# Kernel tuning notes

Measured on AMD Instinct MI355X. Metric: run time of the kernel, lower is better.

The kernel has to match this reference:

```python
import jax, jax.numpy as jnp
import numpy as np

D_MODEL = 1024
N_HEAD = 16
D_HEAD = D_MODEL // N_HEAD
BSZ, QLEN, MLEN = 2, 1024, 1024
KLEN = QLEN + MLEN


def setup_inputs() -> dict:
    key = jax.random.key(0)
    ks = jax.random.split(key, 10)
    s = 1.0 / np.sqrt(D_MODEL)
    inp = {
        "x": jax.random.normal(ks[0], (BSZ, QLEN, D_MODEL), jnp.float32),
        "mem": jax.random.normal(ks[1], (BSZ, MLEN, D_MODEL), jnp.float32),
        "pos_emb": jax.random.normal(ks[2], (KLEN, D_MODEL), jnp.float32),
        # causal mask with memory: query i may attend to key j iff j <= i + MLEN
        "attn_mask": (jnp.arange(KLEN)[None, :] > (jnp.arange(QLEN)[:, None] + MLEN))[None, None],
        "Wq": jax.random.normal(ks[3], (D_MODEL, D_MODEL), jnp.float32) * s,
        "Wk": jax.random.normal(ks[4], (D_MODEL, D_MODEL), jnp.float32) * s,
        "Wv": jax.random.normal(ks[5], (D_MODEL, D_MODEL), jnp.float32) * s,
        "Wr": jax.random.normal(ks[6], (D_MODEL, D_MODEL), jnp.float32) * s,
        "Wo": jax.random.normal(ks[7], (D_MODEL, D_MODEL), jnp.float32) * s,
        "r_w_bias": jax.random.normal(ks[8], (N_HEAD, D_HEAD), jnp.float32) * 0.02,
        "r_r_bias": jax.random.normal(ks[9], (N_HEAD, D_HEAD), jnp.float32) * 0.02,
    }
    return inp


def _rel_shift(x):
    # x: [b, n, q, k]
    b, n, q, k = x.shape
    x_padded = jnp.pad(x, ((0, 0), (0, 0), (0, 0), (1, 0)))  # zero column at front
    x_padded = x_padded.reshape(b, n, k + 1, q)
    return x_padded[:, :, 1:].reshape(b, n, q, k)


def reference(x, mem, pos_emb, attn_mask, Wq, Wk, Wv, Wr, Wo, r_w_bias, r_r_bias):
    bsz, qlen, _ = x.shape
    k_input = jnp.concatenate([mem, x], axis=1)
    klen = k_input.shape[1]
    scale = 1.0 / np.sqrt(D_HEAD)

    # projections -> [b, n, len, d]
    q = jnp.einsum('bqe,de->bqd', x, Wq).reshape(bsz, qlen, N_HEAD, D_HEAD).transpose(0, 2, 1, 3)
    k = jnp.einsum('bke,de->bkd', k_input, Wk).reshape(bsz, klen, N_HEAD, D_HEAD).transpose(0, 2, 1, 3)
    v = jnp.einsum('bke,de->bkd', k_input, Wv).reshape(bsz, klen, N_HEAD, D_HEAD).transpose(0, 2, 1, 3)
    r = jnp.einsum('ke,de->kd', pos_emb, Wr).reshape(klen, N_HEAD, D_HEAD).transpose(1, 0, 2)  # [n,k,d]

    AC = jnp.einsum('bnqd,bnkd->bnqk', q + r_w_bias[None, :, None, :], k)
    BD = jnp.einsum('bnqd,nkd->bnqk', q + r_r_bias[None, :, None, :], r)
    BD = _rel_shift(BD)

    attn_score = (AC + BD) * scale
    attn_score = jnp.where(attn_mask, -jnp.inf, attn_score)
    attn_prob = jax.nn.softmax(attn_score, axis=-1)

    attn_vec = jnp.einsum('bnqk,bnkd->bnqd', attn_prob, v)
    attn_vec = attn_vec.transpose(0, 2, 1, 3).reshape(bsz, qlen, N_HEAD * D_HEAD)
    return jnp.einsum('bqd,ed->bqe', attn_vec, Wo)
```

## Files before the change

kernel.cpp:

```cpp
#include <hip/hip_runtime.h>


#define B_SZ 2
#define QLEN 1024
#define MLEN 1024
#define KLEN 2048
#define DMODEL 1024
#define NH 16
#define DH 64

typedef _Float16 f16;
typedef __attribute__((ext_vector_type(8))) _Float16 f16x8;
typedef __attribute__((ext_vector_type(4))) _Float16 f16x4;
typedef __attribute__((ext_vector_type(4))) float f32x4;

__device__ __forceinline__ f16 f2h(float v) { return (f16)v; }
__device__ __forceinline__ float h2f(f16 v) { return (float)v; }

__device__ __forceinline__ f32x4 mfma16(f16x8 a, f16x8 b, f32x4 c) {
  return __builtin_amdgcn_mfma_f32_16x16x32_f16(a, b, c, 0, 0, 0);
}

__device__ __forceinline__ void gload_lds16(const f16* g, f16* l) {
  __builtin_amdgcn_global_load_lds(
      (const __attribute__((address_space(1))) void*)g,
      (__attribute__((address_space(3))) void*)l, 16, 0, 0);
}

__device__ __forceinline__ float bperm(int srclane, float v) {
  return __int_as_float(
      __builtin_amdgcn_ds_bpermute(srclane << 2, __float_as_int(v)));
}

__global__ __launch_bounds__(256) void convert_kernel(const float* __restrict__ src,
                                                      f16* __restrict__ dst, int n4) {
  const int i = blockIdx.x * 256 + threadIdx.x;
  if (i >= n4) return;
  const float4 v = reinterpret_cast<const float4*>(src)[i];
  f16x4 o = {(f16)v.x, (f16)v.y, (f16)v.z, (f16)v.w};
  reinterpret_cast<f16x4*>(dst)[i] = o;
}

__global__ __launch_bounds__(256) void pack_weights_kernel(
    const float* __restrict__ Wq, const float* __restrict__ Wk,
    const float* __restrict__ Wv, const float* __restrict__ Wr,
    const float* __restrict__ Wo, f16* __restrict__ Wqb, f16* __restrict__ Wkb,
    f16* __restrict__ Wvb, f16* __restrict__ Wrb, f16* __restrict__ Wob) {
  const float* src;
  f16* dst;
  switch (blockIdx.y) {
    case 0: src = Wq; dst = Wqb; break;
    case 1: src = Wk; dst = Wkb; break;
    case 2: src = Wv; dst = Wvb; break;
    case 3: src = Wr; dst = Wrb; break;
    default: src = Wo; dst = Wob; break;
  }
  const int i = blockIdx.x * 256 + threadIdx.x;
  const float4 v = reinterpret_cast<const float4*>(src)[i];
  f16x4 o = {(f16)v.x, (f16)v.y, (f16)v.z, (f16)v.w};
  reinterpret_cast<f16x4*>(dst)[i] = o;
}

__global__ __launch_bounds__(256) void build_kin_kernel(const float* __restrict__ x,
                                                        const float* __restrict__ mem,
                                                        f16* __restrict__ kin,
                                                        f16* __restrict__ xb) {
  const int i = blockIdx.x * 256 + threadIdx.x;
  const int per_b = KLEN * DMODEL / 4;
  const int b = i / per_b;
  const int rem = i - b * per_b;
  const int row = rem / (DMODEL / 4);
  const int cc = (rem - row * (DMODEL / 4)) * 4;
  const float* src = (row < MLEN)
      ? mem + ((size_t)b * MLEN + row) * DMODEL + cc
      : x + ((size_t)b * QLEN + (row - MLEN)) * DMODEL + cc;
  const float4 v = *reinterpret_cast<const float4*>(src);
  f16x4 o = {(f16)v.x, (f16)v.y, (f16)v.z, (f16)v.w};
  *reinterpret_cast<f16x4*>(kin + (size_t)i * 4) = o;
  if (row >= MLEN)
    *reinterpret_cast<f16x4*>(&xb[((size_t)b * QLEN + (row - MLEN)) * DMODEL + cc]) = o;
}

template <int DUAL, int OUT_F32>
__device__ __forceinline__ void gemm_core(const f16* __restrict__ A,
                                          const f16* __restrict__ Bm,
                                          void* __restrict__ C0v,
                                          void* __restrict__ C1v,
                                          const float* __restrict__ bias0,
                                          const float* __restrict__ bias1, int bm,
                                          int bn) {
  const int tid = threadIdx.x;
  const int wave = tid >> 6, lane = tid & 63;
  const int wr = wave >> 1, wc = wave & 1;
  const int lr = lane & 15, hi = lane >> 4;

  __shared__ f16 As[128 * 64];
  __shared__ f16 Bs[128 * 64];

  f32x4 acc[4][4];
#pragma unroll
  for (int m = 0; m < 4; ++m)
#pragma unroll
    for (int n = 0; n < 4; ++n) acc[m][n] = f32x4{0.f, 0.f, 0.f, 0.f};

  for (int k0 = 0; k0 < DMODEL; k0 += 64) {
    __syncthreads();
#pragma unroll
    for (int it = 0; it < 4; ++it) {
      const int c = it * 256 + tid;
      const int row = c >> 3, c16 = c & 7;
      const int c16s = c16 ^ (row & 7);
      gload_lds16(&A[(size_t)(bm + row) * DMODEL + k0 + c16s * 8], &As[c * 8]);
      gload_lds16(&Bm[(size_t)(bn + row) * DMODEL + k0 + c16s * 8], &Bs[c * 8]);
    }
    __syncthreads();
#pragma unroll
    for (int kk = 0; kk < 2; ++kk) {
      f16x8 af[4], bf[4];
#pragma unroll
      for (int m = 0; m < 4; ++m) {
        const int row = wr * 64 + m * 16 + lr;
        const int colf = (kk * 32 + hi * 8) ^ ((row & 7) << 3);
        af[m] = *reinterpret_cast<const f16x8*>(&As[row * 64 + colf]);
      }
#pragma unroll
      for (int n = 0; n < 4; ++n) {
        const int row = wc * 64 + n * 16 + lr;
        const int colf = (kk * 32 + hi * 8) ^ ((row & 7) << 3);
        bf[n] = *reinterpret_cast<const f16x8*>(&Bs[row * 64 + colf]);
      }
#pragma unroll
      for (int m = 0; m < 4; ++m)
#pragma unroll
        for (int n = 0; n < 4; ++n) acc[m][n] = mfma16(af[m], bf[n], acc[m][n]);
    }
  }

#pragma unroll
  for (int m = 0; m < 4; ++m)
#pragma unroll
    for (int n = 0; n < 4; ++n)
#pragma unroll
      for (int r = 0; r < 4; ++r) {
        const int grow = bm + wr * 64 + m * 16 + hi * 4 + r;
        const int gcol = bn + wc * 64 + n * 16 + lr;
        const float v = acc[m][n][r];
        if constexpr (OUT_F32) {
          reinterpret_cast<float*>(C0v)[(size_t)grow * DMODEL + gcol] = v;
        } else if constexpr (DUAL) {
          reinterpret_cast<f16*>(C0v)[(size_t)grow * DMODEL + gcol] =
              f2h(v + bias0[gcol]);
          reinterpret_cast<f16*>(C1v)[(size_t)grow * DMODEL + gcol] =
              f2h(v + bias1[gcol]);
        } else {
          reinterpret_cast<f16*>(C0v)[(size_t)grow * DMODEL + gcol] = f2h(v);
        }
      }
}

__global__ __launch_bounds__(256) void proj_kernel(
    const f16* __restrict__ Xb, const f16* __restrict__ Kin,
    const f16* __restrict__ Pos, const f16* __restrict__ Wqb,
    const f16* __restrict__ Wkb, const f16* __restrict__ Wvb,
    const f16* __restrict__ Wrb, f16* __restrict__ Qwb, f16* __restrict__ Qrb,
    f16* __restrict__ Kbb, f16* __restrict__ Vbb, f16* __restrict__ Rbb,
    const float* __restrict__ rwb, const float* __restrict__ rrb) {
  const int y = blockIdx.y;
  const int bn = blockIdx.x * 128;
  if (y < 16) {
    gemm_core<1, 0>(Xb, Wqb, Qwb, Qrb, rwb, rrb, y * 128, bn);
  } else if (y < 48) {
    gemm_core<0, 0>(Kin, Wkb, Kbb, nullptr, nullptr, nullptr, (y - 16) * 128, bn);
  } else if (y < 80) {
    gemm_core<0, 0>(Kin, Wvb, Vbb, nullptr, nullptr, nullptr, (y - 48) * 128, bn);
  } else {
    gemm_core<0, 0>(Pos, Wrb, Rbb, nullptr, nullptr, nullptr, (y - 80) * 128, bn);
  }
}

__global__ __launch_bounds__(256) void gemm_out_kernel(const f16* __restrict__ A,
                                                       const f16* __restrict__ Bm,
                                                       float* __restrict__ C) {
  gemm_core<0, 1>(A, Bm, C, nullptr, nullptr, nullptr, blockIdx.y * 128,
                  blockIdx.x * 128);
}

__global__ __launch_bounds__(512) void attn_kernel(
    const f16* __restrict__ Qw, const f16* __restrict__ Qr,
    const f16* __restrict__ Kb, const f16* __restrict__ Vb,
    const f16* __restrict__ Rb, float* __restrict__ Opart,
    float2* __restrict__ MLp) {
  const int qi = blockIdx.x >> 1, half = blockIdx.x & 1;
  const int qb = qi * 128;
  const int n = blockIdx.y;
  const int b = blockIdx.z;
  const int tid = threadIdx.x;
  const int wave = tid >> 6, lane = tid & 63;
  const int lr = lane & 15, hi = lane >> 4;
  const int t0 = hi * 4;
  const int w0 = qb + wave * 16;

  const int T = (qb + 128 + MLEN) >> 6;
  const int jt_beg = half ? (T >> 1) : 0;
  const int jt_end = half ? T : (T >> 1);

  __shared__ f16 Ks[64][72];
  __shared__ f16 Vs[64][72];
  __shared__ f16 Ps[8][16][72];

  f16x8 qw[2], qr[2];
  {
    const size_t qbase = ((size_t)(b * QLEN + w0 + lr)) * DMODEL + n * DH;
#pragma unroll
    for (int kk = 0; kk < 2; ++kk) {
      qw[kk] = *reinterpret_cast<const f16x8*>(&Qw[qbase + kk * 32 + hi * 8]);
      qr[kk] = *reinterpret_cast<const f16x8*>(&Qr[qbase + kk * 32 + hi * 8]);
    }
  }

  f32x4 o[4];
#pragma unroll
  for (int df = 0; df < 4; ++df) o[df] = f32x4{0.f, 0.f, 0.f, 0.f};
  float mrow[4], lrow[4];
#pragma unroll
  for (int r = 0; r < 4; ++r) { mrow[r] = -1e30f; lrow[r] = 0.f; }

  const f16* Rn = Rb + n * DH;

  const int krow = tid >> 3, kc8 = (tid & 7) << 3;
  const int vrow = tid & 63, vc8 = ((tid >> 6) & 7) << 3;
  f16x8 kreg, vreg;
  auto issue = [&](int jt) {
    const size_t kvb = ((size_t)(b * KLEN + (jt << 6))) * DMODEL + n * DH;
    kreg = *reinterpret_cast<const f16x8*>(&Kb[kvb + (size_t)krow * DMODEL + kc8]);
    vreg = *reinterpret_cast<const f16x8*>(&Vb[kvb + (size_t)vrow * DMODEL + vc8]);
  };
  auto commit = [&]() {
    *reinterpret_cast<f16x8*>(&Ks[krow][kc8]) = kreg;
#pragma unroll
    for (int e = 0; e < 8; ++e) Vs[vc8 + e][vrow] = vreg[e];
  };

  issue(jt_beg);
  commit();
  __syncthreads();

  for (int jt = jt_beg; jt < jt_end; ++jt) {
    const bool hn = (jt + 1 < jt_end);
    if (hn) issue(jt + 1);

    const int j0 = jt << 6;

    f32x4 s[4];
#pragma unroll
    for (int nf = 0; nf < 4; ++nf) s[nf] = f32x4{0.f, 0.f, 0.f, 0.f};
#pragma unroll
    for (int kk = 0; kk < 2; ++kk)
#pragma unroll
      for (int nf = 0; nf < 4; ++nf) {
        const f16x8 kf =
            *reinterpret_cast<const f16x8*>(&Ks[nf * 16 + lr][kk * 32 + hi * 8]);
        s[nf] = mfma16(qw[kk], kf, s[nf]);
      }

    const int u0 = j0 + QLEN - 16 - w0;
    f32x4 bd[5];
#pragma unroll
    for (int nt = 0; nt < 5; ++nt) bd[nt] = f32x4{0.f, 0.f, 0.f, 0.f};
#pragma unroll
    for (int nt = 0; nt < 5; ++nt) {
      const int u = u0 + nt * 16 + lr;
      const int uc = u < KLEN ? u : KLEN - 1;
#pragma unroll
      for (int kk = 0; kk < 2; ++kk) {
        const f16x8 rf = *reinterpret_cast<const f16x8*>(
            &Rn[(size_t)uc * DMODEL + kk * 32 + hi * 8]);
        bd[nt] = mfma16(qr[kk], rf, bd[nt]);
      }
    }

#pragma unroll
    for (int r = 0; r < 4; ++r) {
      const int off = 15 - t0 - r;
      const int sl = lr + off;
      const int srclane = hi * 16 + (sl & 15);
      const bool cross = sl >= 16;
      const int i = w0 + t0 + r;
#pragma unroll
      for (int nf = 0; nf < 4; ++nf) {
        const float x0 = bperm(srclane, bd[nf][r]);
        const float x1 = bperm(srclane, bd[nf + 1][r]);
        const float bv = cross ? x1 : x0;
        const int j = j0 + nf * 16 + lr;
        s[nf][r] = (j <= i + MLEN) ? (s[nf][r] + bv) * 0.125f : -1e30f;
      }
    }

#pragma unroll
    for (int r = 0; r < 4; ++r) {
      float tmax = fmaxf(fmaxf(s[0][r], s[1][r]), fmaxf(s[2][r], s[3][r]));
#pragma unroll
      for (int d = 1; d < 16; d <<= 1) tmax = fmaxf(tmax, __shfl_xor(tmax, d, 64));
      const float mnew = fmaxf(mrow[r], tmax);
      const float alpha = __expf(mrow[r] - mnew);
      mrow[r] = mnew;
      float tsum = 0.f;
#pragma unroll
      for (int nf = 0; nf < 4; ++nf) {
        const float p = __expf(s[nf][r] - mnew);
        s[nf][r] = p;
        tsum += p;
      }
#pragma unroll
      for (int d = 1; d < 16; d <<= 1) tsum += __shfl_xor(tsum, d, 64);
      lrow[r] = lrow[r] * alpha + tsum;
#pragma unroll
      for (int df = 0; df < 4; ++df) o[df][r] *= alpha;
    }

#pragma unroll
    for (int nf = 0; nf < 4; ++nf)
#pragma unroll
      for (int r = 0; r < 4; ++r) Ps[wave][t0 + r][nf * 16 + lr] = f2h(s[nf][r]);

#pragma unroll
    for (int kk = 0; kk < 2; ++kk) {
      const f16x8 pa =
          *reinterpret_cast<const f16x8*>(&Ps[wave][lr][kk * 32 + hi * 8]);
#pragma unroll
      for (int df = 0; df < 4; ++df) {
        const f16x8 vb =
            *reinterpret_cast<const f16x8*>(&Vs[df * 16 + lr][kk * 32 + hi * 8]);
        o[df] = mfma16(pa, vb, o[df]);
      }
    }

    __syncthreads();
    if (hn) commit();
    __syncthreads();
  }

  const size_t obase =
      (((size_t)(half * B_SZ + b) * NH + n) * QLEN + w0 + t0) * DH;
#pragma unroll
  for (int df = 0; df < 4; ++df)
#pragma unroll
    for (int r = 0; r < 4; ++r)
      Opart[obase + (size_t)r * DH + df * 16 + lr] = o[df][r];
  if (lr == 0) {
    const size_t mbase = ((size_t)(half * B_SZ + b) * NH + n) * QLEN + w0 + t0;
#pragma unroll
    for (int r = 0; r < 4; ++r) MLp[mbase + r] = float2{mrow[r], lrow[r]};
  }
}

__global__ __launch_bounds__(256) void combine_kernel(const float* __restrict__ Op,
                                                      const float2* __restrict__ ML,
                                                      f16* __restrict__ AV) {
  const int idx = blockIdx.x * 256 + threadIdx.x;
  const int d4 = idx & 15;
  const int i = (idx >> 4) & 1023;
  const int n = (idx >> 14) & 15;
  const int b = idx >> 18;
  const size_t r0 = ((size_t)(b * NH + n)) * QLEN + i;
  const size_t r1 = ((size_t)((B_SZ + b) * NH + n)) * QLEN + i;
  const float2 ml0 = ML[r0], ml1 = ML[r1];
  const float M = fmaxf(ml0.x, ml1.x);
  const float e0 = __expf(ml0.x - M), e1 = __expf(ml1.x - M);
  const float inv = 1.f / (ml0.y * e0 + ml1.y * e1);
  const float4 o0 = *reinterpret_cast<const float4*>(&Op[r0 * DH + d4 * 4]);
  const float4 o1 = *reinterpret_cast<const float4*>(&Op[r1 * DH + d4 * 4]);
  f16x4 out;
  out[0] = f2h((o0.x * e0 + o1.x * e1) * inv);
  out[1] = f2h((o0.y * e0 + o1.y * e1) * inv);
  out[2] = f2h((o0.z * e0 + o1.z * e1) * inv);
  out[3] = f2h((o0.w * e0 + o1.w * e1) * inv);
  *reinterpret_cast<f16x4*>(&AV[((size_t)(b * QLEN + i)) * DMODEL + n * DH + d4 * 4]) =
      out;
}

extern "C" void kernel_launch(void* const* d_in, const int* in_sizes, int n_in,
                              void* d_out, int out_size, void* d_ws, size_t ws_size,
                              hipStream_t stream) {
  (void)in_sizes; (void)n_in; (void)out_size; (void)ws_size;
  const float* x   = (const float*)d_in[0];
  const float* mem = (const float*)d_in[1];
  const float* pos = (const float*)d_in[2];
  const float* Wq  = (const float*)d_in[4];
  const float* Wk  = (const float*)d_in[5];
  const float* Wv  = (const float*)d_in[6];
  const float* Wr  = (const float*)d_in[7];
  const float* Wo  = (const float*)d_in[8];
  const float* rwb = (const float*)d_in[9];
  const float* rrb = (const float*)d_in[10];
  float* out = (float*)d_out;

  char* ws = (char*)d_ws;
  size_t off = 0;
  auto alloc = [&](size_t bytes) {
    void* p = (void*)(ws + off);
    off += (bytes + 255) & ~(size_t)255;
    return p;
  };
  f16* Xb  = (f16*)alloc((size_t)B_SZ * QLEN * DMODEL * 2);
  f16* Kin = (f16*)alloc((size_t)B_SZ * KLEN * DMODEL * 2);
  f16* Pos = (f16*)alloc((size_t)KLEN * DMODEL * 2);
  f16* Wqb = (f16*)alloc((size_t)DMODEL * DMODEL * 2);
  f16* Wkb = (f16*)alloc((size_t)DMODEL * DMODEL * 2);
  f16* Wvb = (f16*)alloc((size_t)DMODEL * DMODEL * 2);
  f16* Wrb = (f16*)alloc((size_t)DMODEL * DMODEL * 2);
  f16* Wob = (f16*)alloc((size_t)DMODEL * DMODEL * 2);
  f16* Qwb = (f16*)alloc((size_t)B_SZ * QLEN * DMODEL * 2);
  f16* Qrb = (f16*)alloc((size_t)B_SZ * QLEN * DMODEL * 2);
  f16* Kbb = (f16*)alloc((size_t)B_SZ * KLEN * DMODEL * 2);
  f16* Vbb = (f16*)alloc((size_t)B_SZ * KLEN * DMODEL * 2);
  f16* Rbb = (f16*)alloc((size_t)KLEN * DMODEL * 2);
  f16* AVb = (f16*)alloc((size_t)B_SZ * QLEN * DMODEL * 2);
  float*  Opart = (float*)alloc((size_t)2 * B_SZ * NH * QLEN * DH * 4);
  float2* MLp   = (float2*)alloc((size_t)2 * B_SZ * NH * QLEN * 8);

  pack_weights_kernel<<<dim3(1024, 5), dim3(256), 0, stream>>>(
      Wq, Wk, Wv, Wr, Wo, Wqb, Wkb, Wvb, Wrb, Wob);
  convert_kernel<<<dim3(KLEN * DMODEL / 4 / 256), dim3(256), 0, stream>>>(
      pos, Pos, KLEN * DMODEL / 4);
  build_kin_kernel<<<dim3(B_SZ * KLEN * DMODEL / 4 / 256), dim3(256), 0, stream>>>(
      x, mem, Kin, Xb);

  proj_kernel<<<dim3(8, 96), dim3(256), 0, stream>>>(
      Xb, Kin, Pos, Wqb, Wkb, Wvb, Wrb, Qwb, Qrb, Kbb, Vbb, Rbb, rwb, rrb);

  attn_kernel<<<dim3(QLEN / 128 * 2, NH, B_SZ), dim3(512), 0, stream>>>(
      Qwb, Qrb, Kbb, Vbb, Rbb, Opart, MLp);

  combine_kernel<<<dim3(B_SZ * NH * QLEN * (DH / 4) / 256), dim3(256), 0, stream>>>(
      Opart, MLp, AVb);

  gemm_out_kernel<<<dim3(DMODEL / 128, B_SZ * QLEN / 128), dim3(256), 0, stream>>>(
      AVb, Wob, out);
}
```

Baseline: 281.2 us.

## Split attention key range four ways with XCD-aware block mapping

Splits each query tile's key range into four partial-softmax chunks instead of two, giving 1024 attention blocks, and remaps the flat block index so each head/batch group stays on one XCD for L2 reuse of K/V/R. The combine kernel merges four partial results. The 1/sqrt(d) scale is folded into the Q projection epilogue, which removes a multiply from the score loop. The cost is more partial-output traffic and more per-block Q loading and setup.

```diff
diff --git a/kernel.cpp b/kernel.cpp
--- a/kernel.cpp
+++ b/kernel.cpp
@@ -8,6 +8,7 @@
 #define DMODEL 1024
 #define NH 16
 #define DH 64
+#define NSPLIT 4
 
 typedef _Float16 f16;
 typedef __attribute__((ext_vector_type(8))) _Float16 f16x8;
@@ -149,9 +150,9 @@
           reinterpret_cast<float*>(C0v)[(size_t)grow * DMODEL + gcol] = v;
         } else if constexpr (DUAL) {
           reinterpret_cast<f16*>(C0v)[(size_t)grow * DMODEL + gcol] =
-              f2h(v + bias0[gcol]);
+              f2h((v + bias0[gcol]) * 0.125f);
           reinterpret_cast<f16*>(C1v)[(size_t)grow * DMODEL + gcol] =
-              f2h(v + bias1[gcol]);
+              f2h((v + bias1[gcol]) * 0.125f);
         } else {
           reinterpret_cast<f16*>(C0v)[(size_t)grow * DMODEL + gcol] = f2h(v);
         }
@@ -190,10 +191,14 @@
     const f16* __restrict__ Kb, const f16* __restrict__ Vb,
     const f16* __restrict__ Rb, float* __restrict__ Opart,
     float2* __restrict__ MLp) {
-  const int qi = blockIdx.x >> 1, half = blockIdx.x & 1;
+  const int bid = blockIdx.x;
+  const int xcd = bid & 7, rr = bid >> 3;
+  const int grp = xcd * 4 + (rr >> 5);
+  const int ii = rr & 31;
+  const int b = grp >> 4, n = grp & 15;
+  const int qi = ii >> 2, split = ii & 3;
+
   const int qb = qi * 128;
-  const int n = blockIdx.y;
-  const int b = blockIdx.z;
   const int tid = threadIdx.x;
   const int wave = tid >> 6, lane = tid & 63;
   const int lr = lane & 15, hi = lane >> 4;
@@ -201,8 +206,8 @@
   const int w0 = qb + wave * 16;
 
   const int T = (qb + 128 + MLEN) >> 6;
-  const int jt_beg = half ? (T >> 1) : 0;
-  const int jt_end = half ? T : (T >> 1);
+  const int jt_beg = (split * T) >> 2;
+  const int jt_end = ((split + 1) * T) >> 2;
 
   __shared__ f16 Ks[64][72];
   __shared__ f16 Vs[64][72];
@@ -292,7 +297,7 @@
         const float x1 = bperm(srclane, bd[nf + 1][r]);
         const float bv = cross ? x1 : x0;
         const int j = j0 + nf * 16 + lr;
-        s[nf][r] = (j <= i + MLEN) ? (s[nf][r] + bv) * 0.125f : -1e30f;
+        s[nf][r] = (j <= i + MLEN) ? (s[nf][r] + bv) : -1e30f;
       }
     }
 
@@ -341,14 +346,14 @@
   }
 
   const size_t obase =
-      (((size_t)(half * B_SZ + b) * NH + n) * QLEN + w0 + t0) * DH;
+      (((size_t)(split * B_SZ + b) * NH + n) * QLEN + w0 + t0) * DH;
 #pragma unroll
   for (int df = 0; df < 4; ++df)
 #pragma unroll
     for (int r = 0; r < 4; ++r)
       Opart[obase + (size_t)r * DH + df * 16 + lr] = o[df][r];
   if (lr == 0) {
-    const size_t mbase = ((size_t)(half * B_SZ + b) * NH + n) * QLEN + w0 + t0;
+    const size_t mbase = ((size_t)(split * B_SZ + b) * NH + n) * QLEN + w0 + t0;
 #pragma unroll
     for (int r = 0; r < 4; ++r) MLp[mbase + r] = float2{mrow[r], lrow[r]};
   }
@@ -362,21 +367,39 @@
   const int i = (idx >> 4) & 1023;
   const int n = (idx >> 14) & 15;
   const int b = idx >> 18;
-  const size_t r0 = ((size_t)(b * NH + n)) * QLEN + i;
-  const size_t r1 = ((size_t)((B_SZ + b) * NH + n)) * QLEN + i;
-  const float2 ml0 = ML[r0], ml1 = ML[r1];
-  const float M = fmaxf(ml0.x, ml1.x);
-  const float e0 = __expf(ml0.x - M), e1 = __expf(ml1.x - M);
-  const float inv = 1.f / (ml0.y * e0 + ml1.y * e1);
-  const float4 o0 = *reinterpret_cast<const float4*>(&Op[r0 * DH + d4 * 4]);
-  const float4 o1 = *reinterpret_cast<const float4*>(&Op[r1 * DH + d4 * 4]);
-  f16x4 out;
-  out[0] = f2h((o0.x * e0 + o1.x * e1) * inv);
-  out[1] = f2h((o0.y * e0 + o1.y * e1) * inv);
-  out[2] = f2h((o0.z * e0 + o1.z * e1) * inv);
-  out[3] = f2h((o0.w * e0 + o1.w * e1) * inv);
+  size_t rs[NSPLIT];
+  float2 ml[NSPLIT];
+#pragma unroll
+  for (int s = 0; s < NSPLIT; ++s) {
+    rs[s] = ((size_t)((s * B_SZ + b) * NH + n)) * QLEN + i;
+    ml[s] = ML[rs[s]];
+  }
+  float M = ml[0].x;
+#pragma unroll
+  for (int s = 1; s < NSPLIT; ++s) M = fmaxf(M, ml[s].x);
+  float es[NSPLIT], l = 0.f;
+#pragma unroll
+  for (int s = 0; s < NSPLIT; ++s) {
+    es[s] = __expf(ml[s].x - M);
+    l += ml[s].y * es[s];
+  }
+  const float inv = 1.f / l;
+  float4 acc = {0.f, 0.f, 0.f, 0.f};
+#pragma unroll
+  for (int s = 0; s < NSPLIT; ++s) {
+    const float4 ov = *reinterpret_cast<const float4*>(&Op[rs[s] * DH + d4 * 4]);
+    acc.x += ov.x * es[s];
+    acc.y += ov.y * es[s];
+    acc.z += ov.z * es[s];
+    acc.w += ov.w * es[s];
+  }
+  f16x4 outv;
+  outv[0] = f2h(acc.x * inv);
+  outv[1] = f2h(acc.y * inv);
+  outv[2] = f2h(acc.z * inv);
+  outv[3] = f2h(acc.w * inv);
   *reinterpret_cast<f16x4*>(&AV[((size_t)(b * QLEN + i)) * DMODEL + n * DH + d4 * 4]) =
-      out;
+      outv;
 }
 
 extern "C" void kernel_launch(void* const* d_in, const int* in_sizes, int n_in,
@@ -416,8 +439,8 @@
   f16* Vbb = (f16*)alloc((size_t)B_SZ * KLEN * DMODEL * 2);
   f16* Rbb = (f16*)alloc((size_t)KLEN * DMODEL * 2);
   f16* AVb = (f16*)alloc((size_t)B_SZ * QLEN * DMODEL * 2);
-  float*  Opart = (float*)alloc((size_t)2 * B_SZ * NH * QLEN * DH * 4);
-  float2* MLp   = (float2*)alloc((size_t)2 * B_SZ * NH * QLEN * 8);
+  float*  Opart = (float*)alloc((size_t)NSPLIT * B_SZ * NH * QLEN * DH * 4);
+  float2* MLp   = (float2*)alloc((size_t)NSPLIT * B_SZ * NH * QLEN * 8);
 
   pack_weights_kernel<<<dim3(1024, 5), dim3(256), 0, stream>>>(
       Wq, Wk, Wv, Wr, Wo, Wqb, Wkb, Wvb, Wrb, Wob);
@@ -429,7 +452,7 @@
   proj_kernel<<<dim3(8, 96), dim3(256), 0, stream>>>(
       Xb, Kin, Pos, Wqb, Wkb, Wvb, Wrb, Qwb, Qrb, Kbb, Vbb, Rbb, rwb, rrb);
 
-  attn_kernel<<<dim3(QLEN / 128 * 2, NH, B_SZ), dim3(512), 0, stream>>>(
+  attn_kernel<<<dim3(QLEN / 128 * NSPLIT * NH * B_SZ), dim3(512), 0, stream>>>(
       Qwb, Qrb, Kbb, Vbb, Rbb, Opart, MLp);
 
   combine_kernel<<<dim3(B_SZ * NH * QLEN * (DH / 4) / 256), dim3(256), 0, stream>>>(
```

Measured after the change: 281.6 us. Within noise of the previous version (+0.1%).
